# Performance work log

Measured on AMD Instinct MI355X. Metric: run time of the kernel, lower is better.

Reference implementation:

```python
import jax, jax.numpy as jnp
import numpy as np

B, D, P, C = 4096, 512, 256, 8
LAMBDA = 1.0


def setup_inputs() -> dict:
    key = jax.random.key(0)
    k1, k2, k3, k4 = jax.random.split(key, 4)
    x = jax.random.normal(k1, (B, D), dtype=jnp.float32)
    y = jax.random.randint(k2, (B,), 0, C, dtype=jnp.int32)
    prototypes = jax.random.normal(k3, (P, D), dtype=jnp.float32)
    # omega initialized as eye + 0.01*randn per class, like the torch module
    omega = jnp.eye(D, dtype=jnp.float32)[None] + 0.01 * jax.random.normal(k4, (C, D, D), dtype=jnp.float32)
    prototype_labels = (jnp.arange(P, dtype=jnp.int32) % C).astype(jnp.int32)
    return {"x": x, "y": y, "prototypes": prototypes, "omega": omega, "prototype_labels": prototype_labels}


def reference(x, y, prototypes, omega, prototype_labels):
    # transformed inputs per class: tx[c,b,:] = omega[c] @ x[b]
    tx = jnp.einsum('cij,bj->cbi', omega, x)                     # [C,B,D]
    # transformed prototypes under every class omega, then pick each
    # prototype's own class matrix: tp[p,:] = omega[label[p]] @ w[p]
    tp_all = jnp.einsum('cij,pj->cpi', omega, prototypes)        # [C,P,D]
    tp = tp_all[prototype_labels, jnp.arange(P)]                 # [P,D]
    # squared distances via expansion ||a-b||^2 = |a|^2 + |b|^2 - 2ab
    dots = jnp.einsum('cbd,pd->cbp', tx, tp)                     # [C,B,P]
    x2 = jnp.sum(tx * tx, axis=-1)                               # [C,B]
    p2 = jnp.sum(tp * tp, axis=-1)                               # [P]
    dist_all = x2[:, :, None] + p2[None, None, :] - 2.0 * dots   # [C,B,P]
    # each prototype uses the omega of its own class
    dist = dist_all[prototype_labels, :, jnp.arange(P)].T        # [B,P]
    same = prototype_labels[None, :] == y[:, None]               # [B,P]
    inf = jnp.float32(jnp.inf)
    pos = jnp.min(jnp.where(same, dist, inf), axis=1)            # [B]
    neg = jnp.min(jnp.where(same, inf, dist), axis=1)            # [B]
    mu = (pos - neg) / (pos + neg)
    loss = jnp.mean(jax.nn.sigmoid(LAMBDA * mu))
    loss = loss + 0.01 * jnp.linalg.norm(omega.reshape(-1))
    return loss
```

## Files before the change

kernel.cpp:

```cpp
#include <hip/hip_runtime.h>
#include <math.h>

typedef unsigned short ushort_t;
typedef __attribute__((ext_vector_type(8))) short short8;
typedef __attribute__((ext_vector_type(4))) float f32x4;

#define B_N 4096
#define D_N 512
#define P_N 256
#define C_N 8

#define ACC_OFF   0
#define P2G_OFF   256
#define X2_OFF    1280
#define XB_OFF    132352
#define OMB_OFF   (XB_OFF + B_N*D_N*2)
#define TPG_OFF   (OMB_OFF + C_N*D_N*D_N*2)
#define UG_OFF    (TPG_OFF + P_N*D_N*2)
#define OMBT_OFF  (UG_OFF + P_N*D_N*2)
#define MINB_OFF  OMBT_OFF

#define MFMA16(a, b, c) __builtin_amdgcn_mfma_f32_16x16x32_bf16(a, b, c, 0, 0, 0)

__device__ inline ushort_t f2bf(float f) {
    union { float f; unsigned u; } v; v.f = f;
    unsigned r = v.u + 0x7FFFu + ((v.u >> 16) & 1u);
    return (ushort_t)(r >> 16);
}

__device__ __forceinline__ void gll16(const ushort_t* g, ushort_t* l) {
    __builtin_amdgcn_global_load_lds((const __attribute__((address_space(1))) void*)g,
                                     (__attribute__((address_space(3))) void*)l, 16, 0, 0);
}

__global__ void k_cast_x(const float* __restrict__ x, ushort_t* __restrict__ xb) {
    int idx = blockIdx.x * 256 + threadIdx.x;
    const float4* x4 = (const float4*)x;
    float4 a = x4[idx * 2], b = x4[idx * 2 + 1];
    union { ushort_t s[8]; uint4 v; } o;
    o.s[0] = f2bf(a.x); o.s[1] = f2bf(a.y); o.s[2] = f2bf(a.z); o.s[3] = f2bf(a.w);
    o.s[4] = f2bf(b.x); o.s[5] = f2bf(b.y); o.s[6] = f2bf(b.z); o.s[7] = f2bf(b.w);
    ((uint4*)xb)[idx] = o.v;
}

__global__ void k_cast_om(const float* __restrict__ omega, ushort_t* __restrict__ omb,
                          ushort_t* __restrict__ ombT, float* __restrict__ oss) {
    int c = blockIdx.z, r0 = blockIdx.y * 64, c0 = blockIdx.x * 64;
    __shared__ ushort_t T[64][72];
    __shared__ float red[4];
    int t = threadIdx.x;
    int r = t >> 2, seg = t & 3;
    const float* src = omega + ((size_t)c * D_N + r0 + r) * D_N + c0 + seg * 16;
    float4 v0 = ((const float4*)src)[0], v1 = ((const float4*)src)[1];
    float4 v2 = ((const float4*)src)[2], v3 = ((const float4*)src)[3];
    float s = v0.x*v0.x + v0.y*v0.y + v0.z*v0.z + v0.w*v0.w
            + v1.x*v1.x + v1.y*v1.y + v1.z*v1.z + v1.w*v1.w
            + v2.x*v2.x + v2.y*v2.y + v2.z*v2.z + v2.w*v2.w
            + v3.x*v3.x + v3.y*v3.y + v3.z*v3.z + v3.w*v3.w;
    union { ushort_t s[16]; uint4 v[2]; } o;
    float vv[16] = {v0.x,v0.y,v0.z,v0.w, v1.x,v1.y,v1.z,v1.w,
                    v2.x,v2.y,v2.z,v2.w, v3.x,v3.y,v3.z,v3.w};
    #pragma unroll
    for (int j = 0; j < 16; ++j) o.s[j] = f2bf(vv[j]);
    uint4* dst = (uint4*)(omb + ((size_t)c * D_N + r0 + r) * D_N + c0 + seg * 16);
    dst[0] = o.v[0]; dst[1] = o.v[1];
    #pragma unroll
    for (int j = 0; j < 16; ++j) T[seg * 16 + j][r] = o.s[j];
    __syncthreads();
    int jr = t >> 2, sg2 = t & 3;
    uint4 w0 = *(uint4*)&T[jr][sg2 * 16];
    uint4 w1 = *(uint4*)&T[jr][sg2 * 16 + 8];
    uint4* dstT = (uint4*)(ombT + ((size_t)c * D_N + c0 + jr) * D_N + r0 + sg2 * 16);
    dstT[0] = w0; dstT[1] = w1;
    #pragma unroll
    for (int off = 32; off > 0; off >>= 1) s += __shfl_down(s, off);
    if ((t & 63) == 0) red[t >> 6] = s;
    __syncthreads();
    if (t == 0) atomicAdd(oss, red[0] + red[1] + red[2] + red[3]);
}

__global__ __launch_bounds__(256) void k_tp(const float* __restrict__ prot,
                                            const ushort_t* __restrict__ omb,
                                            ushort_t* __restrict__ tpg,
                                            float* __restrict__ p2g) {
    int i0 = blockIdx.x * 64, c = blockIdx.y;
    __shared__ ushort_t As[32][72];
    __shared__ ushort_t Bs[64][72];
    int t = threadIdx.x, w = t >> 6, lane = t & 63;
    int g = lane >> 4, cl = lane & 15;
    f32x4 acc[2] = {{0,0,0,0},{0,0,0,0}};
    for (int k0 = 0; k0 < D_N; k0 += 64) {
        __syncthreads();
        {
            int m = t >> 3, seg = t & 7;
            const float* ap = prot + ((size_t)(c + 8 * m)) * D_N + k0 + seg * 8;
            float4 u0 = ((const float4*)ap)[0], u1 = ((const float4*)ap)[1];
            union { ushort_t s[8]; uint4 v; } o;
            o.s[0]=f2bf(u0.x); o.s[1]=f2bf(u0.y); o.s[2]=f2bf(u0.z); o.s[3]=f2bf(u0.w);
            o.s[4]=f2bf(u1.x); o.s[5]=f2bf(u1.y); o.s[6]=f2bf(u1.z); o.s[7]=f2bf(u1.w);
            *(uint4*)&As[m][seg * 8] = o.v;
        }
        {
            int r = t >> 2, sg = t & 3;
            const uint4* bp = (const uint4*)(omb + ((size_t)c * D_N + i0 + r) * D_N + k0 + sg * 16);
            *(uint4*)&Bs[r][sg * 16] = bp[0];
            *(uint4*)&Bs[r][sg * 16 + 8] = bp[1];
        }
        __syncthreads();
        #pragma unroll
        for (int kk = 0; kk < 2; ++kk) {
            int koff = kk * 32 + g * 8;
            short8 bfr = *(const short8*)&Bs[w * 16 + cl][koff];
            #pragma unroll
            for (int mt = 0; mt < 2; ++mt) {
                short8 afr = *(const short8*)&As[mt * 16 + cl][koff];
                acc[mt] = MFMA16(afr, bfr, acc[mt]);
            }
        }
    }
    #pragma unroll
    for (int mt = 0; mt < 2; ++mt)
        #pragma unroll
        for (int reg = 0; reg < 4; ++reg) {
            float v = acc[mt][reg];
            int m = mt * 16 + g * 4 + reg;
            int i = i0 + w * 16 + cl;
            tpg[((size_t)c * 32 + m) * D_N + i] = f2bf(v);
            float s = v * v;
            s += __shfl_xor(s, 1); s += __shfl_xor(s, 2);
            s += __shfl_xor(s, 4); s += __shfl_xor(s, 8);
            if (cl == 0) atomicAdd(&p2g[c * 32 + m], s);
        }
}

__global__ __launch_bounds__(256) void k_u(const ushort_t* __restrict__ tpg,
                                           const ushort_t* __restrict__ ombT,
                                           ushort_t* __restrict__ ug) {
    int j0 = blockIdx.x * 64, c = blockIdx.y;
    __shared__ ushort_t As[32][72];
    __shared__ ushort_t Bs[64][72];
    int t = threadIdx.x, w = t >> 6, lane = t & 63;
    int g = lane >> 4, cl = lane & 15;
    f32x4 acc[2] = {{0,0,0,0},{0,0,0,0}};
    for (int k0 = 0; k0 < D_N; k0 += 64) {
        __syncthreads();
        {
            int m = t >> 3, seg = t & 7;
            *(uint4*)&As[m][seg * 8] =
                *(const uint4*)(tpg + ((size_t)c * 32 + m) * D_N + k0 + seg * 8);
        }
        {
            int r = t >> 2, sg = t & 3;
            const uint4* bp = (const uint4*)(ombT + ((size_t)c * D_N + j0 + r) * D_N + k0 + sg * 16);
            *(uint4*)&Bs[r][sg * 16] = bp[0];
            *(uint4*)&Bs[r][sg * 16 + 8] = bp[1];
        }
        __syncthreads();
        #pragma unroll
        for (int kk = 0; kk < 2; ++kk) {
            int koff = kk * 32 + g * 8;
            short8 bfr = *(const short8*)&Bs[w * 16 + cl][koff];
            #pragma unroll
            for (int mt = 0; mt < 2; ++mt) {
                short8 afr = *(const short8*)&As[mt * 16 + cl][koff];
                acc[mt] = MFMA16(afr, bfr, acc[mt]);
            }
        }
    }
    #pragma unroll
    for (int mt = 0; mt < 2; ++mt)
        #pragma unroll
        for (int reg = 0; reg < 4; ++reg) {
            int m = mt * 16 + g * 4 + reg;
            int j = j0 + w * 16 + cl;
            ug[((size_t)c * 32 + m) * D_N + j] = f2bf(acc[mt][reg]);
        }
}

__global__ __launch_bounds__(256, 4) void k_x2d(const ushort_t* __restrict__ xb,
                                                const ushort_t* __restrict__ omb,
                                                const ushort_t* __restrict__ ug,
                                                const float* __restrict__ p2g,
                                                float* __restrict__ x2,
                                                float* __restrict__ minb) {
    int c  = blockIdx.y;
    int b0 = blockIdx.z * 128;
    int t = threadIdx.x, w = t >> 6, lane = t & 63;
    int g = lane >> 4, cl = lane & 15;
    int srow = lane >> 2, spos = lane & 3;

    __shared__ ushort_t Xs[2][128][32];
    __shared__ ushort_t Os[2][128][32];
    __shared__ float red[128][2];

    if (blockIdx.x < 4) {
        int i0 = blockIdx.x * 128;
        int qr = w >> 1, qc = w & 1;
        f32x4 acc[4][4];
        #pragma unroll
        for (int mt = 0; mt < 4; ++mt)
            #pragma unroll
            for (int nt = 0; nt < 4; ++nt) acc[mt][nt] = (f32x4){0,0,0,0};
        #pragma unroll
        for (int i = 0; i < 2; ++i) {
            int rb = w * 32 + i * 16;
            int r  = rb + srow;
            int cg = (spos + r) & 3;
            gll16(xb + (size_t)(b0 + r) * D_N + cg * 8, &Xs[0][rb][0]);
            gll16(omb + ((size_t)c * D_N + i0 + r) * D_N + cg * 8, &Os[0][rb][0]);
        }
        __syncthreads();
        for (int s = 0; s < 16; ++s) {
            int cb = s & 1, nb = cb ^ 1;
            if (s < 15) {
                int k1 = (s + 1) * 32;
                #pragma unroll
                for (int i = 0; i < 2; ++i) {
                    int rb = w * 32 + i * 16;
                    int r  = rb + srow;
                    int cg = (spos + r) & 3;
                    gll16(xb + (size_t)(b0 + r) * D_N + k1 + cg * 8, &Xs[nb][rb][0]);
                    gll16(omb + ((size_t)c * D_N + i0 + r) * D_N + k1 + cg * 8, &Os[nb][rb][0]);
                }
            }
            short8 a[4], b[4];
            #pragma unroll
            for (int mt = 0; mt < 4; ++mt) {
                int r = qr * 64 + mt * 16 + cl;
                a[mt] = *(const short8*)&Xs[cb][r][((g - r) & 3) * 8];
            }
            #pragma unroll
            for (int nt = 0; nt < 4; ++nt) {
                int r = qc * 64 + nt * 16 + cl;
                b[nt] = *(const short8*)&Os[cb][r][((g - r) & 3) * 8];
            }
            #pragma unroll
            for (int mt = 0; mt < 4; ++mt)
                #pragma unroll
                for (int nt = 0; nt < 4; ++nt)
                    acc[mt][nt] = MFMA16(a[mt], b[nt], acc[mt][nt]);
            __syncthreads();
        }
        #pragma unroll
        for (int mt = 0; mt < 4; ++mt)
            #pragma unroll
            for (int reg = 0; reg < 4; ++reg) {
                float s = 0.f;
                #pragma unroll
                for (int nt = 0; nt < 4; ++nt) s += acc[mt][nt][reg] * acc[mt][nt][reg];
                s += __shfl_xor(s, 1); s += __shfl_xor(s, 2);
                s += __shfl_xor(s, 4); s += __shfl_xor(s, 8);
                if (cl == 0) red[qr * 64 + mt * 16 + g * 4 + reg][qc] = s;
            }
        __syncthreads();
        if (t < 128) atomicAdd(&x2[(size_t)(b0 + t) * C_N + c], red[t][0] + red[t][1]);
    } else {
        f32x4 acc[2][2];
        #pragma unroll
        for (int mt = 0; mt < 2; ++mt)
            #pragma unroll
            for (int nt = 0; nt < 2; ++nt) acc[mt][nt] = (f32x4){0,0,0,0};
        #pragma unroll
        for (int i = 0; i < 2; ++i) {
            int rb = w * 32 + i * 16;
            int r  = rb + srow;
            int cg = (spos + r) & 3;
            gll16(xb + (size_t)(b0 + r) * D_N + cg * 8, &Xs[0][rb][0]);
        }
        if (w < 2) {
            int rb = w * 16;
            int r  = rb + srow;
            int cg = (spos + r) & 3;
            gll16(ug + ((size_t)c * 32 + r) * D_N + cg * 8, &Os[0][rb][0]);
        }
        __syncthreads();
        for (int s = 0; s < 16; ++s) {
            int cb = s & 1, nb = cb ^ 1;
            if (s < 15) {
                int k1 = (s + 1) * 32;
                #pragma unroll
                for (int i = 0; i < 2; ++i) {
                    int rb = w * 32 + i * 16;
                    int r  = rb + srow;
                    int cg = (spos + r) & 3;
                    gll16(xb + (size_t)(b0 + r) * D_N + k1 + cg * 8, &Xs[nb][rb][0]);
                }
                if (w < 2) {
                    int rb = w * 16;
                    int r  = rb + srow;
                    int cg = (spos + r) & 3;
                    gll16(ug + ((size_t)c * 32 + r) * D_N + k1 + cg * 8, &Os[nb][rb][0]);
                }
            }
            short8 a[2], b[2];
            #pragma unroll
            for (int mt = 0; mt < 2; ++mt) {
                int r = w * 32 + mt * 16 + cl;
                a[mt] = *(const short8*)&Xs[cb][r][((g - r) & 3) * 8];
            }
            #pragma unroll
            for (int nt = 0; nt < 2; ++nt) {
                int r = nt * 16 + cl;
                b[nt] = *(const short8*)&Os[cb][r][((g - r) & 3) * 8];
            }
            #pragma unroll
            for (int mt = 0; mt < 2; ++mt)
                #pragma unroll
                for (int nt = 0; nt < 2; ++nt)
                    acc[mt][nt] = MFMA16(a[mt], b[nt], acc[mt][nt]);
            __syncthreads();
        }
        #pragma unroll
        for (int mt = 0; mt < 2; ++mt)
            #pragma unroll
            for (int reg = 0; reg < 4; ++reg) {
                float v = INFINITY;
                #pragma unroll
                for (int nt = 0; nt < 2; ++nt) {
                    int q = c * 32 + nt * 16 + cl;
                    v = fminf(v, p2g[q] - 2.f * acc[mt][nt][reg]);
                }
                v = fminf(v, __shfl_xor(v, 1)); v = fminf(v, __shfl_xor(v, 2));
                v = fminf(v, __shfl_xor(v, 4)); v = fminf(v, __shfl_xor(v, 8));
                if (cl == 0)
                    minb[(size_t)(b0 + w * 32 + mt * 16 + g * 4 + reg) * C_N + c] = v;
            }
    }
}

__global__ void k_mu(const float* __restrict__ x2, const float* __restrict__ minb,
                     const int* __restrict__ y, float* __restrict__ acc) {
    int t = threadIdx.x;
    int b = blockIdx.x * 256 + t;
    int yb = y[b];
    float d[8];
    #pragma unroll
    for (int cc = 0; cc < 8; ++cc)
        d[cc] = x2[(size_t)b * C_N + cc] + minb[(size_t)b * C_N + cc];
    float pos = d[yb];
    float neg = INFINITY;
    #pragma unroll
    for (int cc = 0; cc < 8; ++cc)
        if (cc != yb) neg = fminf(neg, d[cc]);
    float mu = (pos - neg) / (pos + neg);
    float s = 1.f / (1.f + expf(-mu));
    #pragma unroll
    for (int off = 32; off > 0; off >>= 1) s += __shfl_down(s, off);
    __shared__ float red[4];
    if ((t & 63) == 0) red[t >> 6] = s;
    __syncthreads();
    if (t == 0) atomicAdd(acc, red[0] + red[1] + red[2] + red[3]);
}

__global__ void k_final(const float* __restrict__ accs, float* __restrict__ out) {
    out[0] = accs[0] * (1.f / (float)B_N) + 0.01f * sqrtf(accs[1]);
}

extern "C" void kernel_launch(void* const* d_in, const int* in_sizes, int n_in,
                              void* d_out, int out_size, void* d_ws, size_t ws_size,
                              hipStream_t stream) {
    (void)in_sizes; (void)n_in; (void)out_size; (void)ws_size;
    const float* x     = (const float*)d_in[0];
    const int*   y     = (const int*)d_in[1];
    const float* prot  = (const float*)d_in[2];
    const float* omega = (const float*)d_in[3];

    char* ws = (char*)d_ws;
    float*    accs = (float*)(ws + ACC_OFF);
    float*    p2g  = (float*)(ws + P2G_OFF);
    float*    x2   = (float*)(ws + X2_OFF);
    ushort_t* xb   = (ushort_t*)(ws + XB_OFF);
    ushort_t* omb  = (ushort_t*)(ws + OMB_OFF);
    ushort_t* tpg  = (ushort_t*)(ws + TPG_OFF);
    ushort_t* ug   = (ushort_t*)(ws + UG_OFF);
    ushort_t* ombT = (ushort_t*)(ws + OMBT_OFF);
    float*    minb = (float*)(ws + MINB_OFF);

    (void)hipMemsetAsync(ws, 0, XB_OFF, stream);
    k_cast_x <<<B_N * D_N / 8 / 256, 256, 0, stream>>>(x, xb);
    k_cast_om<<<dim3(8, 8, C_N), 256, 0, stream>>>(omega, omb, ombT, accs + 1);
    k_tp     <<<dim3(8, C_N), 256, 0, stream>>>(prot, omb, tpg, p2g);
    k_u      <<<dim3(8, C_N), 256, 0, stream>>>(tpg, ombT, ug);
    k_x2d    <<<dim3(5, C_N, B_N / 128), 256, 0, stream>>>(xb, omb, ug, p2g, x2, minb);
    k_mu     <<<B_N / 256, 256, 0, stream>>>(x2, minb, y, accs);
    k_final  <<<1, 1, 0, stream>>>(accs, (float*)d_out);
}
```

Baseline: 133.8 us.

## Merge cast kernels, widen x2 GEMM tile, fold final reduction into k_mu

Merges the x and omega cast kernels into a single launch and folds the final scalar computation into k_mu using a last-block counter, removing two kernel launches. Widens the x2 GEMM tile in k_x2d from 128x128 to 128x256 (acc[4][8]), halving how often each X tile is reloaded. Launch bounds drop to 2 blocks per CU to leave room for the extra registers. The LDS swizzle changes to a pair-row XOR pattern with a precomputed read offset. The trade-off is more register and LDS pressure and lower occupancy in the main GEMM.

```diff
diff --git a/kernel.cpp b/kernel.cpp
--- a/kernel.cpp
+++ b/kernel.cpp
@@ -33,22 +33,25 @@
                                      (__attribute__((address_space(3))) void*)l, 16, 0, 0);
 }
 
-__global__ void k_cast_x(const float* __restrict__ x, ushort_t* __restrict__ xb) {
-    int idx = blockIdx.x * 256 + threadIdx.x;
-    const float4* x4 = (const float4*)x;
-    float4 a = x4[idx * 2], b = x4[idx * 2 + 1];
-    union { ushort_t s[8]; uint4 v; } o;
-    o.s[0] = f2bf(a.x); o.s[1] = f2bf(a.y); o.s[2] = f2bf(a.z); o.s[3] = f2bf(a.w);
-    o.s[4] = f2bf(b.x); o.s[5] = f2bf(b.y); o.s[6] = f2bf(b.z); o.s[7] = f2bf(b.w);
-    ((uint4*)xb)[idx] = o.v;
-}
-
-__global__ void k_cast_om(const float* __restrict__ omega, ushort_t* __restrict__ omb,
-                          ushort_t* __restrict__ ombT, float* __restrict__ oss) {
-    int c = blockIdx.z, r0 = blockIdx.y * 64, c0 = blockIdx.x * 64;
+__global__ void k_cast(const float* __restrict__ x, const float* __restrict__ omega,
+                       ushort_t* __restrict__ xb, ushort_t* __restrict__ omb,
+                       ushort_t* __restrict__ ombT, float* __restrict__ oss) {
     __shared__ ushort_t T[64][72];
     __shared__ float red[4];
     int t = threadIdx.x;
+    if (blockIdx.x < 1024) {
+        int idx = blockIdx.x * 256 + t;
+        const float4* x4 = (const float4*)x;
+        float4 a = x4[idx * 2], b = x4[idx * 2 + 1];
+        union { ushort_t s[8]; uint4 v; } o;
+        o.s[0] = f2bf(a.x); o.s[1] = f2bf(a.y); o.s[2] = f2bf(a.z); o.s[3] = f2bf(a.w);
+        o.s[4] = f2bf(b.x); o.s[5] = f2bf(b.y); o.s[6] = f2bf(b.z); o.s[7] = f2bf(b.w);
+        ((uint4*)xb)[idx] = o.v;
+        return;
+    }
+    int bid = blockIdx.x - 1024;
+    int c = bid >> 6, by = (bid >> 3) & 7, bx = bid & 7;
+    int r0 = by * 64, c0 = bx * 64;
     int r = t >> 2, seg = t & 3;
     const float* src = omega + ((size_t)c * D_N + r0 + r) * D_N + c0 + seg * 16;
     float4 v0 = ((const float4*)src)[0], v1 = ((const float4*)src)[1];
@@ -177,7 +180,7 @@
         }
 }
 
-__global__ __launch_bounds__(256, 4) void k_x2d(const ushort_t* __restrict__ xb,
+__global__ __launch_bounds__(256, 2) void k_x2d(const ushort_t* __restrict__ xb,
                                                 const ushort_t* __restrict__ omb,
                                                 const ushort_t* __restrict__ ug,
                                                 const float* __restrict__ p2g,
@@ -188,25 +191,32 @@
     int t = threadIdx.x, w = t >> 6, lane = t & 63;
     int g = lane >> 4, cl = lane & 15;
     int srow = lane >> 2, spos = lane & 3;
+    int ch = ((g - (cl >> 1)) & 3) * 8;
 
     __shared__ ushort_t Xs[2][128][32];
-    __shared__ ushort_t Os[2][128][32];
+    __shared__ ushort_t Os[2][256][32];
     __shared__ float red[128][2];
 
-    if (blockIdx.x < 4) {
-        int i0 = blockIdx.x * 128;
+    if (blockIdx.x < 2) {
+        int i0 = blockIdx.x * 256;
         int qr = w >> 1, qc = w & 1;
-        f32x4 acc[4][4];
+        f32x4 acc[4][8];
         #pragma unroll
         for (int mt = 0; mt < 4; ++mt)
             #pragma unroll
-            for (int nt = 0; nt < 4; ++nt) acc[mt][nt] = (f32x4){0,0,0,0};
+            for (int nt = 0; nt < 8; ++nt) acc[mt][nt] = (f32x4){0,0,0,0};
         #pragma unroll
         for (int i = 0; i < 2; ++i) {
             int rb = w * 32 + i * 16;
             int r  = rb + srow;
-            int cg = (spos + r) & 3;
+            int cg = (spos + (r >> 1)) & 3;
             gll16(xb + (size_t)(b0 + r) * D_N + cg * 8, &Xs[0][rb][0]);
+        }
+        #pragma unroll
+        for (int i = 0; i < 4; ++i) {
+            int rb = w * 64 + i * 16;
+            int r  = rb + srow;
+            int cg = (spos + (r >> 1)) & 3;
             gll16(omb + ((size_t)c * D_N + i0 + r) * D_N + cg * 8, &Os[0][rb][0]);
         }
         __syncthreads();
@@ -218,26 +228,28 @@
                 for (int i = 0; i < 2; ++i) {
                     int rb = w * 32 + i * 16;
                     int r  = rb + srow;
-                    int cg = (spos + r) & 3;
+                    int cg = (spos + (r >> 1)) & 3;
                     gll16(xb + (size_t)(b0 + r) * D_N + k1 + cg * 8, &Xs[nb][rb][0]);
+                }
+                #pragma unroll
+                for (int i = 0; i < 4; ++i) {
+                    int rb = w * 64 + i * 16;
+                    int r  = rb + srow;
+                    int cg = (spos + (r >> 1)) & 3;
                     gll16(omb + ((size_t)c * D_N + i0 + r) * D_N + k1 + cg * 8, &Os[nb][rb][0]);
                 }
             }
-            short8 a[4], b[4];
-            #pragma unroll
-            for (int mt = 0; mt < 4; ++mt) {
-                int r = qr * 64 + mt * 16 + cl;
-                a[mt] = *(const short8*)&Xs[cb][r][((g - r) & 3) * 8];
-            }
-            #pragma unroll
-            for (int nt = 0; nt < 4; ++nt) {
-                int r = qc * 64 + nt * 16 + cl;
-                b[nt] = *(const short8*)&Os[cb][r][((g - r) & 3) * 8];
-            }
+            short8 a[4], b[8];
             #pragma unroll
             for (int mt = 0; mt < 4; ++mt)
-                #pragma unroll
-                for (int nt = 0; nt < 4; ++nt)
+                a[mt] = *(const short8*)&Xs[cb][qr * 64 + mt * 16 + cl][ch];
+            #pragma unroll
+            for (int nt = 0; nt < 8; ++nt)
+                b[nt] = *(const short8*)&Os[cb][qc * 128 + nt * 16 + cl][ch];
+            #pragma unroll
+            for (int mt = 0; mt < 4; ++mt)
+                #pragma unroll
+                for (int nt = 0; nt < 8; ++nt)
                     acc[mt][nt] = MFMA16(a[mt], b[nt], acc[mt][nt]);
             __syncthreads();
         }
@@ -247,7 +259,7 @@
             for (int reg = 0; reg < 4; ++reg) {
                 float s = 0.f;
                 #pragma unroll
-                for (int nt = 0; nt < 4; ++nt) s += acc[mt][nt][reg] * acc[mt][nt][reg];
+                for (int nt = 0; nt < 8; ++nt) s += acc[mt][nt][reg] * acc[mt][nt][reg];
                 s += __shfl_xor(s, 1); s += __shfl_xor(s, 2);
                 s += __shfl_xor(s, 4); s += __shfl_xor(s, 8);
                 if (cl == 0) red[qr * 64 + mt * 16 + g * 4 + reg][qc] = s;
@@ -264,13 +276,13 @@
         for (int i = 0; i < 2; ++i) {
             int rb = w * 32 + i * 16;
             int r  = rb + srow;
-            int cg = (spos + r) & 3;
+            int cg = (spos + (r >> 1)) & 3;
             gll16(xb + (size_t)(b0 + r) * D_N + cg * 8, &Xs[0][rb][0]);
         }
         if (w < 2) {
             int rb = w * 16;
             int r  = rb + srow;
-            int cg = (spos + r) & 3;
+            int cg = (spos + (r >> 1)) & 3;
             gll16(ug + ((size_t)c * 32 + r) * D_N + cg * 8, &Os[0][rb][0]);
         }
         __syncthreads();
@@ -282,27 +294,23 @@
                 for (int i = 0; i < 2; ++i) {
                     int rb = w * 32 + i * 16;
                     int r  = rb + srow;
-                    int cg = (spos + r) & 3;
+                    int cg = (spos + (r >> 1)) & 3;
                     gll16(xb + (size_t)(b0 + r) * D_N + k1 + cg * 8, &Xs[nb][rb][0]);
                 }
                 if (w < 2) {
                     int rb = w * 16;
                     int r  = rb + srow;
-                    int cg = (spos + r) & 3;
+                    int cg = (spos + (r >> 1)) & 3;
                     gll16(ug + ((size_t)c * 32 + r) * D_N + k1 + cg * 8, &Os[nb][rb][0]);
                 }
             }
             short8 a[2], b[2];
             #pragma unroll
-            for (int mt = 0; mt < 2; ++mt) {
-                int r = w * 32 + mt * 16 + cl;
-                a[mt] = *(const short8*)&Xs[cb][r][((g - r) & 3) * 8];
-            }
-            #pragma unroll
-            for (int nt = 0; nt < 2; ++nt) {
-                int r = nt * 16 + cl;
-                b[nt] = *(const short8*)&Os[cb][r][((g - r) & 3) * 8];
-            }
+            for (int mt = 0; mt < 2; ++mt)
+                a[mt] = *(const short8*)&Xs[cb][w * 32 + mt * 16 + cl][ch];
+            #pragma unroll
+            for (int nt = 0; nt < 2; ++nt)
+                b[nt] = *(const short8*)&Os[cb][nt * 16 + cl][ch];
             #pragma unroll
             for (int mt = 0; mt < 2; ++mt)
                 #pragma unroll
@@ -329,7 +337,8 @@
 }
 
 __global__ void k_mu(const float* __restrict__ x2, const float* __restrict__ minb,
-                     const int* __restrict__ y, float* __restrict__ acc) {
+                     const int* __restrict__ y, float* __restrict__ accs,
+                     float* __restrict__ out) {
     int t = threadIdx.x;
     int b = blockIdx.x * 256 + t;
     int yb = y[b];
@@ -349,11 +358,16 @@
     __shared__ float red[4];
     if ((t & 63) == 0) red[t >> 6] = s;
     __syncthreads();
-    if (t == 0) atomicAdd(acc, red[0] + red[1] + red[2] + red[3]);
-}
-
-__global__ void k_final(const float* __restrict__ accs, float* __restrict__ out) {
-    out[0] = accs[0] * (1.f / (float)B_N) + 0.01f * sqrtf(accs[1]);
+    if (t == 0) {
+        atomicAdd(accs, red[0] + red[1] + red[2] + red[3]);
+        __threadfence();
+        unsigned n = atomicAdd((unsigned int*)(accs + 2), 1u);
+        if (n == (unsigned)(B_N / 256 - 1)) {
+            float ls  = atomicAdd(accs, 0.f);
+            float oss = atomicAdd(accs + 1, 0.f);
+            out[0] = ls * (1.f / (float)B_N) + 0.01f * sqrtf(oss);
+        }
+    }
 }
 
 extern "C" void kernel_launch(void* const* d_in, const int* in_sizes, int n_in,
@@ -377,11 +391,9 @@
     float*    minb = (float*)(ws + MINB_OFF);
 
     (void)hipMemsetAsync(ws, 0, XB_OFF, stream);
-    k_cast_x <<<B_N * D_N / 8 / 256, 256, 0, stream>>>(x, xb);
-    k_cast_om<<<dim3(8, 8, C_N), 256, 0, stream>>>(omega, omb, ombT, accs + 1);
+    k_cast   <<<1536, 256, 0, stream>>>(x, omega, xb, omb, ombT, accs + 1);
     k_tp     <<<dim3(8, C_N), 256, 0, stream>>>(prot, omb, tpg, p2g);
     k_u      <<<dim3(8, C_N), 256, 0, stream>>>(tpg, ombT, ug);
-    k_x2d    <<<dim3(5, C_N, B_N / 128), 256, 0, stream>>>(xb, omb, ug, p2g, x2, minb);
-    k_mu     <<<B_N / 256, 256, 0, stream>>>(x2, minb, y, accs);
-    k_final  <<<1, 1, 0, stream>>>(accs, (float*)d_out);
-}
+    k_x2d    <<<dim3(3, C_N, B_N / 128), 256, 0, stream>>>(xb, omb, ug, p2g, x2, minb);
+    k_mu     <<<B_N / 256, 256, 0, stream>>>(x2, minb, y, accs, (float*)d_out);
+}
```

After: 137.7 us. 1.03x slower.
